# Kernel optimization log

Hardware: AMD Instinct MI355X
Metric: run time of the kernel (lower is better)

Reference implementation:

```python
import jax, jax.numpy as jnp
import numpy as np

NUM_ITEMS = 10000
EMB_DIM = 32
HIST_LEN = 4_000_000


def setup_inputs() -> dict:
    key = jax.random.key(0)
    k_hist, k_emb = jax.random.split(key)
    user_history = jax.random.randint(k_hist, (HIST_LEN,), 0, NUM_ITEMS, dtype=jnp.int64 if jax.config.jax_enable_x64 else jnp.int32)
    item_embeddings = jax.random.uniform(k_emb, (NUM_ITEMS, EMB_DIM), dtype=jnp.float32)
    return {"user_history": user_history, "item_embeddings": item_embeddings, "k": 10}


def reference(user_history, item_embeddings, k):
    # gather [H, 32] then mean-pool over the history dim -> [32]
    user_embedding = item_embeddings[user_history].mean(axis=0)
    # score every item: [32] @ [32, N] -> [N]
    scores = user_embedding @ item_embeddings.T
    # top-k indices, descending by score (matches torch.topk default)
    _, indices = jax.lax.top_k(scores, k)
    return indices
```

## Files before the change

### kernel.cpp

```cpp
#include <hip/hip_runtime.h>
#include <stdint.h>

#define NITEMS 10000
#define EDIM 32
#define NWORDS 5000

constexpr int NBH = 255;
constexpr int TBH = 1024;
constexpr int NBE = 80;
constexpr int TBE = 256;
constexpr int IPE = NITEMS / NBE;
constexpr int NBS = 40;
constexpr int TBS = 256;
constexpr int IPB = (NITEMS + NBS - 1) / NBS;



__global__ __launch_bounds__(TBH) void k1_hist(
    const int* __restrict__ hist, int H,
    uint32_t* __restrict__ hist_g,
    uint32_t* __restrict__ hist_sum,
    unsigned int* __restrict__ counter)
{
    __shared__ uint32_t cnt[NWORDS];
    for (int i = threadIdx.x; i < NWORDS; i += TBH) cnt[i] = 0;

    if (blockIdx.x == 0) {
        for (int i = threadIdx.x; i < NWORDS; i += TBH) hist_sum[i] = 0;
        if (threadIdx.x == 0) *counter = 0;
    }
    __syncthreads();

    int tid = blockIdx.x * TBH + threadIdx.x;
    int nth = gridDim.x * TBH;
    const int4* h4 = (const int4*)hist;
    int H4 = H >> 2;
    for (int i = tid; i < H4; i += nth) {
        int4 v = h4[i];
        atomicAdd(&cnt[v.x >> 1], 1u << ((v.x & 1) << 4));
        atomicAdd(&cnt[v.y >> 1], 1u << ((v.y & 1) << 4));
        atomicAdd(&cnt[v.z >> 1], 1u << ((v.z & 1) << 4));
        atomicAdd(&cnt[v.w >> 1], 1u << ((v.w & 1) << 4));
    }
    for (int i = (H4 << 2) + tid; i < H; i += nth) {
        int v = hist[i];
        atomicAdd(&cnt[v >> 1], 1u << ((v & 1) << 4));
    }
    __syncthreads();

    uint32_t* dst = hist_g + (size_t)blockIdx.x * NWORDS;
    for (int i = threadIdx.x; i < NWORDS; i += TBH) dst[i] = cnt[i];
}

__global__ __launch_bounds__(128) void k2a_merge(
    const uint32_t* __restrict__ hist_g,
    uint32_t* __restrict__ hist_sum)
{
    int w = blockIdx.x * 128 + threadIdx.x;
    if (w >= NWORDS) return;
    int r0 = blockIdx.y * 32;
    int r1 = r0 + 32; if (r1 > NBH) r1 = NBH;
    uint32_t lo = 0, hi = 0;
    #pragma unroll 8
    for (int r = r0; r < r1; ++r) {
        uint32_t v = hist_g[(size_t)r * NWORDS + w];
        lo += v & 0xFFFFu;
        hi += v >> 16;
    }
    atomicAdd(&hist_sum[w], (hi << 16) | lo);
}

__global__ __launch_bounds__(TBE) void k2b_embsum(
    const uint32_t* __restrict__ hist_sum,
    const float* __restrict__ emb,
    double* __restrict__ partials)
{
    __shared__ double sred[TBE / 32][32];
    int t = threadIdx.x;
    int d = t & 31;
    int g = t >> 5;
    int base = blockIdx.x * IPE;

    double acc = 0.0;
    for (int i = g; i < IPE; i += TBE / 32) {
        int item = base + i;
        uint32_t wv = hist_sum[item >> 1];
        int c = (item & 1) ? (int)(wv >> 16) : (int)(wv & 0xFFFFu);
        acc += (double)c * (double)emb[item * EDIM + d];
    }
    sred[g][d] = acc;
    __syncthreads();
    if (t < 32) {
        double s = sred[0][t];
        #pragma unroll
        for (int g2 = 1; g2 < TBE / 32; ++g2) s += sred[g2][t];
        partials[blockIdx.x * 32 + t] = s;
    }
}


__global__ __launch_bounds__(1024) void k1_fb_hist_embsum(
    const int* __restrict__ hist, int H,
    const float* __restrict__ emb,
    double* __restrict__ partials)
{
    __shared__ int cnt[NITEMS];
    __shared__ double sred[32][32];

    for (int i = threadIdx.x; i < NITEMS; i += 1024) cnt[i] = 0;
    __syncthreads();

    int tid = blockIdx.x * 1024 + threadIdx.x;
    int nth = gridDim.x * 1024;
    const int4* h4 = (const int4*)hist;
    int H4 = H >> 2;
    for (int i = tid; i < H4; i += nth) {
        int4 v = h4[i];
        atomicAdd(&cnt[v.x], 1);
        atomicAdd(&cnt[v.y], 1);
        atomicAdd(&cnt[v.z], 1);
        atomicAdd(&cnt[v.w], 1);
    }
    for (int i = (H4 << 2) + tid; i < H; i += nth) atomicAdd(&cnt[hist[i]], 1);
    __syncthreads();

    int d = threadIdx.x & 31;
    int g = threadIdx.x >> 5;
    double acc = 0.0;
    for (int i = g; i < NITEMS; i += 32)
        acc += (double)cnt[i] * (double)emb[i * EDIM + d];
    sred[g][d] = acc;
    __syncthreads();
    if (threadIdx.x < 32) {
        double s = 0.0;
        #pragma unroll
        for (int g2 = 0; g2 < 32; ++g2) s += sred[g2][threadIdx.x];
        partials[blockIdx.x * 32 + threadIdx.x] = s;
    }
}


__device__ __forceinline__ unsigned long long umax64(unsigned long long a, unsigned long long b) {
    return a > b ? a : b;
}

__device__ __forceinline__ unsigned long long wave_max64(unsigned long long v) {
    #pragma unroll
    for (int off = 32; off > 0; off >>= 1)
        v = umax64(v, __shfl_xor(v, off));
    return v;
}

__global__ __launch_bounds__(TBS) void k3_score_topk(
    const double* __restrict__ partials, int nparts,
    const float* __restrict__ emb,
    double invH,
    unsigned long long* __restrict__ cand,
    unsigned int* __restrict__ counter,
    int* __restrict__ out, int K)
{
    __shared__ double sred[TBS / 32][32];
    __shared__ float um[EDIM];
    __shared__ unsigned long long wred[TBS / 64];
    __shared__ unsigned long long winner;
    __shared__ int lastFlag;

    int t = threadIdx.x;
    int lane = t & 63;
    int wv = t >> 6;
    constexpr int NW = TBS / 64;

    {
        int d = t & 31;
        int g = t >> 5;
        double acc = 0.0;
        for (int b = g; b < nparts; b += TBS / 32)
            acc += partials[b * EDIM + d];
        sred[g][d] = acc;
        __syncthreads();
        if (t < 32) {
            double s = sred[0][t];
            #pragma unroll
            for (int g2 = 1; g2 < TBS / 32; ++g2) s += sred[g2][t];
            um[t] = (float)(s * invH);
        }
        __syncthreads();
    }

    int item = blockIdx.x * IPB + t;
    unsigned long long my = 0ull;
    if (t < IPB && item < NITEMS) {
        const float4* row = (const float4*)(emb + (size_t)item * EDIM);
        float sc = 0.f;
        #pragma unroll
        for (int q = 0; q < EDIM / 4; ++q) {
            float4 v = row[q];
            sc += um[q * 4 + 0] * v.x + um[q * 4 + 1] * v.y
                + um[q * 4 + 2] * v.z + um[q * 4 + 3] * v.w;
        }
        unsigned int sb = __float_as_uint(sc);
        my = ((unsigned long long)sb << 32)
           | (unsigned long long)(0xFFFFFFFFu - (unsigned int)item);
    }

    for (int it = 0; it < K; ++it) {
        unsigned long long w = wave_max64(my);
        if (lane == 0) wred[wv] = w;
        __syncthreads();
        if (t == 0) {
            unsigned long long win = wred[0];
            #pragma unroll
            for (int j = 1; j < NW; ++j) win = umax64(win, wred[j]);
            winner = win;
            __hip_atomic_store(&cand[blockIdx.x * K + it], win,
                               __ATOMIC_RELAXED, __HIP_MEMORY_SCOPE_AGENT);
        }
        __syncthreads();
        if (my == winner) my = 0ull;
    }

    if (t == 0) {
        unsigned int prev = __hip_atomic_fetch_add(counter, 1u,
                               __ATOMIC_ACQ_REL, __HIP_MEMORY_SCOPE_AGENT);
        lastFlag = (prev == (unsigned int)(gridDim.x - 1));
    }
    __syncthreads();
    if (!lastFlag) return;

    int NC = gridDim.x * K;
    unsigned long long a = 0ull, b = 0ull;
    if (t < NC)
        a = __hip_atomic_load(&cand[t], __ATOMIC_RELAXED, __HIP_MEMORY_SCOPE_AGENT);
    if (t + TBS < NC)
        b = __hip_atomic_load(&cand[t + TBS], __ATOMIC_RELAXED, __HIP_MEMORY_SCOPE_AGENT);

    for (int it = 0; it < K; ++it) {
        unsigned long long m = umax64(a, b);
        unsigned long long w = wave_max64(m);
        if (lane == 0) wred[wv] = w;
        __syncthreads();
        if (t == 0) {
            unsigned long long win = wred[0];
            #pragma unroll
            for (int j = 1; j < NW; ++j) win = umax64(win, wred[j]);
            winner = win;
            out[it] = (int)(0xFFFFFFFFu - (unsigned int)(win & 0xFFFFFFFFull));
        }
        __syncthreads();
        unsigned long long win = winner;
        if (a == win) a = 0ull;
        if (b == win) b = 0ull;
    }
}

extern "C" void kernel_launch(void* const* d_in, const int* in_sizes, int n_in,
                              void* d_out, int out_size, void* d_ws, size_t ws_size,
                              hipStream_t stream) {
    const int*   hist = (const int*)d_in[0];
    const float* emb  = (const float*)d_in[1];
    int H = in_sizes[0];
    int K = out_size;
    double invH = 1.0 / (double)H;
    char* ws = (char*)d_ws;

    constexpr size_t FAST_WS = 5120004;

    if (ws_size >= FAST_WS) {
        uint32_t* hist_g         = (uint32_t*)ws;
        uint32_t* hist_sum       = (uint32_t*)(ws + 5100000);
        unsigned int* counter    = (unsigned int*)(ws + 5120000);
        double* partials         = (double*)ws;
        unsigned long long* cand = (unsigned long long*)(ws + 20480);

        hipLaunchKernelGGL(k1_hist, dim3(NBH), dim3(TBH), 0, stream,
                           hist, H, hist_g, hist_sum, counter);
        hipLaunchKernelGGL(k2a_merge, dim3((NWORDS + 127) / 128, 8), dim3(128), 0, stream,
                           hist_g, hist_sum);
        hipLaunchKernelGGL(k2b_embsum, dim3(NBE), dim3(TBE), 0, stream,
                           hist_sum, emb, partials);
        hipLaunchKernelGGL(k3_score_topk, dim3(NBS), dim3(TBS), 0, stream,
                           partials, NBE, emb, invH, cand, counter, (int*)d_out, K);
    } else {
        double* partials         = (double*)ws;
        unsigned int* counter    = (unsigned int*)(ws + 65536);
        unsigned long long* cand = (unsigned long long*)(ws + 65792);

        hipMemsetAsync(counter, 0, sizeof(unsigned int), stream);
        hipLaunchKernelGGL(k1_fb_hist_embsum, dim3(256), dim3(1024), 0, stream,
                           hist, H, emb, partials);
        hipLaunchKernelGGL(k3_score_topk, dim3(NBS), dim3(TBS), 0, stream,
                           partials, 256, emb, invH, cand, counter, (int*)d_out, K);
    }
}
```

Baseline: 34.86 us.

## Fuse histogram merge and embedding weighted-sum into one kernel

Combines the histogram merge kernel and the embedding-sum kernel into one kernel in which each block reduces the per-block histograms for its own slice of words through shared memory, then directly computes the weighted embedding partial sums. This removes one kernel launch, the global atomics into hist_sum, and the zeroing of hist_sum. The workspace layout changes so that partials no longer alias hist_g. Each of the 40 blocks now reads all 256 histogram rows for its slice, and only 40 blocks run, which limits parallelism for the merge.

```diff
diff --git a/kernel.cpp b/kernel.cpp
--- a/kernel.cpp
+++ b/kernel.cpp
@@ -5,11 +5,14 @@
 #define EDIM 32
 #define NWORDS 5000
 
-constexpr int NBH = 255;
+constexpr int NBH = 256;
 constexpr int TBH = 1024;
-constexpr int NBE = 80;
-constexpr int TBE = 256;
-constexpr int IPE = NITEMS / NBE;
+constexpr int NBE = 40;
+constexpr int TBE = 1024;
+constexpr int WPB = NWORDS / NBE;
+constexpr int IPEB = 2 * WPB;
+constexpr int CHUNKS = 8;
+constexpr int RPC = NBH / CHUNKS;
 constexpr int NBS = 40;
 constexpr int TBS = 256;
 constexpr int IPB = (NITEMS + NBS - 1) / NBS;
@@ -19,16 +22,11 @@
 __global__ __launch_bounds__(TBH) void k1_hist(
     const int* __restrict__ hist, int H,
     uint32_t* __restrict__ hist_g,
-    uint32_t* __restrict__ hist_sum,
     unsigned int* __restrict__ counter)
 {
     __shared__ uint32_t cnt[NWORDS];
     for (int i = threadIdx.x; i < NWORDS; i += TBH) cnt[i] = 0;
-
-    if (blockIdx.x == 0) {
-        for (int i = threadIdx.x; i < NWORDS; i += TBH) hist_sum[i] = 0;
-        if (threadIdx.x == 0) *counter = 0;
-    }
+    if (blockIdx.x == 0 && threadIdx.x == 0) *counter = 0;
     __syncthreads();
 
     int tid = blockIdx.x * TBH + threadIdx.x;
@@ -52,41 +50,53 @@
     for (int i = threadIdx.x; i < NWORDS; i += TBH) dst[i] = cnt[i];
 }
 
-__global__ __launch_bounds__(128) void k2a_merge(
+__global__ __launch_bounds__(TBE) void k2_merge_embsum(
     const uint32_t* __restrict__ hist_g,
-    uint32_t* __restrict__ hist_sum)
-{
-    int w = blockIdx.x * 128 + threadIdx.x;
-    if (w >= NWORDS) return;
-    int r0 = blockIdx.y * 32;
-    int r1 = r0 + 32; if (r1 > NBH) r1 = NBH;
-    uint32_t lo = 0, hi = 0;
-    #pragma unroll 8
-    for (int r = r0; r < r1; ++r) {
-        uint32_t v = hist_g[(size_t)r * NWORDS + w];
-        lo += v & 0xFFFFu;
-        hi += v >> 16;
-    }
-    atomicAdd(&hist_sum[w], (hi << 16) | lo);
-}
-
-__global__ __launch_bounds__(TBE) void k2b_embsum(
-    const uint32_t* __restrict__ hist_sum,
     const float* __restrict__ emb,
     double* __restrict__ partials)
 {
+    __shared__ uint32_t partLo[CHUNKS][WPB + 3];
+    __shared__ uint32_t partHi[CHUNKS][WPB + 3];
+    __shared__ int cnt[IPEB];
     __shared__ double sred[TBE / 32][32];
+
     int t = threadIdx.x;
+    int w_idx = t & 127;
+    int chunk = t >> 7;
+    int wbase = blockIdx.x * WPB;
+
+    if (w_idx < WPB) {
+        uint32_t lo = 0, hi = 0;
+        const uint32_t* src = hist_g + (size_t)(chunk * RPC) * NWORDS + wbase + w_idx;
+        #pragma unroll 8
+        for (int r = 0; r < RPC; ++r) {
+            uint32_t v = src[(size_t)r * NWORDS];
+            lo += v & 0xFFFFu;
+            hi += v >> 16;
+        }
+        partLo[chunk][w_idx] = lo;
+        partHi[chunk][w_idx] = hi;
+    }
+    __syncthreads();
+
+    if (t < WPB) {
+        uint32_t lo = 0, hi = 0;
+        #pragma unroll
+        for (int c = 0; c < CHUNKS; ++c) {
+            lo += partLo[c][t];
+            hi += partHi[c][t];
+        }
+        cnt[2 * t]     = (int)lo;
+        cnt[2 * t + 1] = (int)hi;
+    }
+    __syncthreads();
+
     int d = t & 31;
     int g = t >> 5;
-    int base = blockIdx.x * IPE;
-
+    int ibase = blockIdx.x * IPEB;
     double acc = 0.0;
-    for (int i = g; i < IPE; i += TBE / 32) {
-        int item = base + i;
-        uint32_t wv = hist_sum[item >> 1];
-        int c = (item & 1) ? (int)(wv >> 16) : (int)(wv & 0xFFFFu);
-        acc += (double)c * (double)emb[item * EDIM + d];
+    for (int i = g; i < IPEB; i += TBE / 32) {
+        acc += (double)cnt[i] * (double)emb[(ibase + i) * EDIM + d];
     }
     sred[g][d] = acc;
     __syncthreads();
@@ -263,21 +273,18 @@
     double invH = 1.0 / (double)H;
     char* ws = (char*)d_ws;
 
-    constexpr size_t FAST_WS = 5120004;
+    constexpr size_t FAST_WS = 5133696;
 
     if (ws_size >= FAST_WS) {
         uint32_t* hist_g         = (uint32_t*)ws;
-        uint32_t* hist_sum       = (uint32_t*)(ws + 5100000);
-        unsigned int* counter    = (unsigned int*)(ws + 5120000);
-        double* partials         = (double*)ws;
-        unsigned long long* cand = (unsigned long long*)(ws + 20480);
+        double* partials         = (double*)(ws + 5120000);
+        unsigned int* counter    = (unsigned int*)(ws + 5130240);
+        unsigned long long* cand = (unsigned long long*)(ws + 5130496);
 
         hipLaunchKernelGGL(k1_hist, dim3(NBH), dim3(TBH), 0, stream,
-                           hist, H, hist_g, hist_sum, counter);
-        hipLaunchKernelGGL(k2a_merge, dim3((NWORDS + 127) / 128, 8), dim3(128), 0, stream,
-                           hist_g, hist_sum);
-        hipLaunchKernelGGL(k2b_embsum, dim3(NBE), dim3(TBE), 0, stream,
-                           hist_sum, emb, partials);
+                           hist, H, hist_g, counter);
+        hipLaunchKernelGGL(k2_merge_embsum, dim3(NBE), dim3(TBE), 0, stream,
+                           hist_g, emb, partials);
         hipLaunchKernelGGL(k3_score_topk, dim3(NBS), dim3(TBS), 0, stream,
                            partials, NBE, emb, invH, cand, counter, (int*)d_out, K);
     } else {
```

Result: faster. 29.12 us, median of 2 (-16.5%).
